# Kernel tuning notes

Hardware: AMD Instinct MI355X
Metric: run time of the kernel (lower is better)

Reference implementation:

```python
import math
import jax, jax.numpy as jnp
import numpy as np

EMB = 1024
HEADS = 16
HD = EMB // HEADS  # 64
MAXPOS = 1024
BATCH = 4
SEQ = 1024


def get_rope_cache(dim, max_pos, theta=10000.0):
    # NOTE: faithfully reproduces the (i - 1) quirk of the source (not the standard i)
    i = jnp.arange(dim // 2, dtype=jnp.float32)
    theta_i = theta ** (-2.0 * (i - 1.0) / dim)
    pos = jnp.arange(max_pos, dtype=jnp.float32)[:, None]
    th = pos * theta_i  # [max_pos, dim//2]
    return jnp.stack([jnp.cos(th), jnp.sin(th)], axis=-1)  # [max_pos, dim//2, 2]


def apply_rope(x, rope_cache):
    # x: [B, H, S, hd]. Source casts pairs to float16 before the complex multiply,
    # then the complex32*complex64 product promotes back to float32 -> emulate via
    # an fp16 round-trip on x, with the rotation itself done in fp32.
    B, H, S, hd = x.shape
    rc = rope_cache[:S]  # [S, hd//2, 2]
    xp = x.reshape(B, H, S, hd // 2, 2).astype(jnp.float16).astype(jnp.float32)
    a, b = xp[..., 0], xp[..., 1]
    cos, sin = rc[..., 0], rc[..., 1]
    rot = jnp.stack([a * cos - b * sin, a * sin + b * cos], axis=-1)
    return rot.reshape(B, H, S, hd)


def setup_inputs() -> dict:
    key = jax.random.key(0)
    ks = jax.random.split(key, 5)
    std = math.sqrt(2.0 / (EMB + EMB))
    x = jax.random.normal(ks[0], (BATCH, SEQ, EMB), dtype=jnp.float32)
    padding_mask = jnp.ones((BATCH, SEQ), dtype=jnp.float32)
    Wq = jax.random.normal(ks[1], (EMB, EMB), dtype=jnp.float32) * std
    Wk = jax.random.normal(ks[2], (EMB, EMB), dtype=jnp.float32) * std
    Wv = jax.random.normal(ks[3], (EMB, EMB), dtype=jnp.float32) * std
    Wo = jax.random.normal(ks[4], (EMB, EMB), dtype=jnp.float32) * std
    rope_cache = get_rope_cache(HD, MAXPOS)
    return {"x": x, "padding_mask": padding_mask, "Wq": Wq, "Wk": Wk,
            "Wv": Wv, "Wo": Wo, "rope_cache": rope_cache}


def reference(x, padding_mask, Wq, Wk, Wv, Wo, rope_cache):
    B, S, E = x.shape

    def heads(t):  # [B,S,E] -> [B,H,S,hd]
        return t.reshape(B, S, HEADS, HD).transpose(0, 2, 1, 3)

    q = heads(x @ Wq.T)
    k = heads(x @ Wk.T)
    v = heads(x @ Wv.T)
    q = apply_rope(q, rope_cache)
    k = apply_rope(k, rope_cache)

    scores = jnp.einsum('bhqd,bhkd->bhqk', q, k)  # [B,H,S,S]
    causal = jnp.tril(jnp.ones((S, S), jnp.float32))
    mask = (causal[None, :, :] * padding_mask[:, None, :])[:, None]  # [B,1,S,S]
    scores = jnp.where(mask == 0, jnp.float32(-1e9), scores) / math.sqrt(HD)
    weights = jax.nn.softmax(scores, axis=-1)

    out = jnp.einsum('bhqk,bhkd->bhqd', weights, v)  # [B,H,S,hd]
    # Faithful to source: transpose(-2,-1) then .view(B,S,-1) scrambles head_dim/seq
    out = out.transpose(0, 1, 3, 2).reshape(B, S, E)
    return out @ Wo.T
```

## Files before the change

kernel.cpp:

```cpp
#include <hip/hip_runtime.h>

#define SEQ   1024
#define HEADS 16
#define HD    64
#define BATCH 4
#define EMB   1024

typedef __attribute__((ext_vector_type(8))) short  short8;
typedef __attribute__((ext_vector_type(4))) float  floatx4;

__device__ __forceinline__ unsigned short f2bf(float f) {
    unsigned u = __builtin_bit_cast(unsigned, f);
    u += 0x7FFF + ((u >> 16) & 1);
    return (unsigned short)(u >> 16);
}

__device__ __forceinline__ void g2l16(const void* g, void* l) {
    __builtin_amdgcn_global_load_lds((const __attribute__((address_space(1))) unsigned int*)g,
                                     (__attribute__((address_space(3))) unsigned int*)l,
                                     16, 0, 0);
}

__device__ __forceinline__ short8 ldsfrag(const unsigned short* base, int row, int cq) {
    int ch = cq ^ (row & 7);
    return *(const short8*)(base + row * 64 + ch * 8);
}

__global__ __launch_bounds__(256) void cvt_kernel(
    const float* __restrict__ x,  const float* __restrict__ wq,
    const float* __restrict__ wk, const float* __restrict__ wv,
    const float* __restrict__ wo,
    unsigned short* __restrict__ xb,  unsigned short* __restrict__ wqb,
    unsigned short* __restrict__ wkb, unsigned short* __restrict__ wvb,
    unsigned short* __restrict__ wob) {
    int blk = blockIdx.x;
    const float* src; unsigned short* dst; int rel;
    if      (blk < 4096) { src = x;  dst = xb;  rel = blk; }
    else if (blk < 5120) { src = wq; dst = wqb; rel = blk - 4096; }
    else if (blk < 6144) { src = wk; dst = wkb; rel = blk - 5120; }
    else if (blk < 7168) { src = wv; dst = wvb; rel = blk - 6144; }
    else                 { src = wo; dst = wob; rel = blk - 7168; }
    size_t i = (size_t)rel * 1024 + threadIdx.x * 4;
    float4 v = *(const float4*)(src + i);
    ushort4 o;
    o.x = f2bf(v.x); o.y = f2bf(v.y); o.z = f2bf(v.z); o.w = f2bf(v.w);
    *(ushort4*)(dst + i) = o;
}

template<int MODE>
__global__ __launch_bounds__(256) void gemm_m97(
    const unsigned short* __restrict__ A, const unsigned short* __restrict__ W,
    void* __restrict__ out0, void* __restrict__ out1, void* __restrict__ out2,
    const float* __restrict__ rc, int M, int N, int K) {
    __shared__ unsigned short As[128 * 64];
    __shared__ unsigned short Bs[128 * 64];
    const int tid  = threadIdx.x;
    const int lane = tid & 63;
    const int wid  = tid >> 6;
    const int l15  = lane & 15, quad = lane >> 4;
    const int wm   = (wid & 1) * 64, wn = (wid >> 1) * 64;
    const int m0   = blockIdx.y * 128, n0 = blockIdx.x * 128;
    const int boff = tid * 16;

    floatx4 acc[4][4] = {};
    const char* Ab = (const char*)A;
    const char* Wb = (const char*)W;
    const size_t rstride = (size_t)K * 2;

    for (int k0 = 0; k0 < K; k0 += 64) {
#pragma unroll
        for (int c = 0; c < 4; c++) {
            int o = c * 4096 + boff;
            int row = o >> 7;
            int sw  = ((o >> 4) & 7) ^ (row & 7);
            g2l16(Ab + (size_t)(m0 + row) * rstride + (size_t)k0 * 2 + sw * 16, (char*)As + o);
            g2l16(Wb + (size_t)(n0 + row) * rstride + (size_t)k0 * 2 + sw * 16, (char*)Bs + o);
        }
        __syncthreads();
#pragma unroll
        for (int ks = 0; ks < 2; ks++) {
            short8 a[4], b[4];
#pragma unroll
            for (int i = 0; i < 4; i++) a[i] = ldsfrag(As, wm + i * 16 + l15, ks * 4 + quad);
#pragma unroll
            for (int j = 0; j < 4; j++) b[j] = ldsfrag(Bs, wn + j * 16 + l15, ks * 4 + quad);
#pragma unroll
            for (int i = 0; i < 4; i++)
#pragma unroll
                for (int j = 0; j < 4; j++)
                    acc[i][j] = __builtin_amdgcn_mfma_f32_16x16x32_bf16(a[i], b[j], acc[i][j], 0, 0, 0);
        }
        __syncthreads();
    }

    const int which = n0 >> 10;
#pragma unroll
    for (int i = 0; i < 4; i++) {
#pragma unroll
        for (int r = 0; r < 4; r++) {
            int m = m0 + wm + i * 16 + quad * 4 + r;
            int bb = m >> 10, s = m & 1023;
#pragma unroll
            for (int j = 0; j < 4; j++) {
                int n = n0 + wn + j * 16 + l15;
                float v = acc[i][j][r];
                if (MODE == 0) {
                    ((float*)out0)[(size_t)m * N + n] = v;
                } else {
                    int nr = n & 1023, h = nr >> 6, d = nr & 63;
                    if (which < 2) {
                        float vp = __shfl_xor(v, 1);
                        float2 cs = *(const float2*)&rc[(size_t)s * 64 + (d & ~1)];
                        v = (l15 & 1) ? (vp * cs.y + v * cs.x) : (v * cs.x - vp * cs.y);
                        unsigned short* dst = (which == 0) ? (unsigned short*)out0
                                                           : (unsigned short*)out1;
                        dst[(((size_t)bb * HEADS + h) * SEQ + s) * HD + d] = f2bf(v);
                    } else {
                        ((unsigned short*)out2)[(((size_t)bb * HEADS + h) * HD + d) * SEQ + s] = f2bf(v);
                    }
                }
            }
        }
    }
}

__global__ __launch_bounds__(256) void attn_kernel(
    const unsigned short* __restrict__ Qb, const unsigned short* __restrict__ Kb,
    const unsigned short* __restrict__ VTb, const float* __restrict__ pm,
    unsigned short* __restrict__ Tb) {
    __shared__ unsigned short Ks[64 * 64];
    __shared__ unsigned short Vs[64 * 64];
    __shared__ unsigned short Ps[4][16][72];
    __shared__ float pmf[64];
    const int tid  = threadIdx.x;
    const int lane = tid & 63, wid = tid >> 6;
    const int l15  = lane & 15, quad = lane >> 4;
    const int bh   = blockIdx.x, b = bh >> 4;
    const int q0   = (15 - blockIdx.y) * 64;
    const int qw   = q0 + wid * 16;
    const int q    = qw + l15;
    const unsigned short* Qh  = Qb  + (size_t)bh * SEQ * HD;
    const unsigned short* Kh  = Kb  + (size_t)bh * SEQ * HD;
    const unsigned short* VTh = VTb + (size_t)bh * HD * SEQ;
    unsigned short*       Th  = Tb  + (size_t)bh * HD * SEQ;
    const float* pmb = pm + b * SEQ;
    const float SCL2 = 0.125f * 1.44269504088896340736f;

    short8 qf0 = *(const short8*)&Qh[(size_t)q * HD + quad * 8];
    short8 qf1 = *(const short8*)&Qh[(size_t)q * HD + 32 + quad * 8];

    floatx4 ot[4] = {};
    float l_lane = 0.f;
    unsigned short (*Pw)[72] = Ps[wid];
    const int boff = tid * 16;

    for (int kvc = 0; kvc <= q0; kvc += 64) {
        const char* kg = (const char*)(Kh + (size_t)kvc * HD);
        const char* vg = (const char*)(VTh + kvc);
#pragma unroll
        for (int c = 0; c < 2; c++) {
            int o = c * 4096 + boff;
            int row = o >> 7;
            int sw  = ((o >> 4) & 7) ^ (row & 7);
            g2l16(kg + (size_t)row * 128 + sw * 16, (char*)Ks + o);
            g2l16(vg + (size_t)row * (SEQ * 2) + sw * 16, (char*)Vs + o);
        }
        if (tid < 64) pmf[tid] = (pmb[kvc + tid] != 0.f) ? 1.f : 0.f;
        __syncthreads();

        const bool diag = (kvc + 63 > qw);
        floatx4 sc[4];
#pragma unroll
        for (int st = 0; st < 4; st++) {
            short8 ka0 = ldsfrag(Ks, st * 16 + l15, quad);
            short8 ka1 = ldsfrag(Ks, st * 16 + l15, 4 + quad);
            floatx4 z = {0.f, 0.f, 0.f, 0.f};
            z = __builtin_amdgcn_mfma_f32_16x16x32_bf16(ka0, qf0, z, 0, 0, 0);
            z = __builtin_amdgcn_mfma_f32_16x16x32_bf16(ka1, qf1, z, 0, 0, 0);
            sc[st] = z;
        }
#pragma unroll
        for (int st = 0; st < 4; st++) {
            float4 pmv = *(const float4*)&pmf[st * 16 + quad * 4];
            int kvbase = kvc + st * 16 + quad * 4;
            ushort4 pk;
#pragma unroll
            for (int r = 0; r < 4; r++) {
                float e = exp2f(sc[st][r] * SCL2) * ((&pmv.x)[r]);
                if (diag && (kvbase + r > q)) e = 0.f;
                l_lane += e;
                (&pk.x)[r] = f2bf(e);
            }
            *(ushort4*)&Pw[l15][st * 16 + quad * 4] = pk;
        }
        asm volatile("s_waitcnt lgkmcnt(0)" ::: "memory");
        short8 pf0 = *(const short8*)&Pw[l15][quad * 8];
        short8 pf1 = *(const short8*)&Pw[l15][32 + quad * 8];

#pragma unroll
        for (int jt = 0; jt < 4; jt++) {
            short8 v0 = ldsfrag(Vs, jt * 16 + l15, quad);
            short8 v1 = ldsfrag(Vs, jt * 16 + l15, 4 + quad);
            ot[jt] = __builtin_amdgcn_mfma_f32_16x16x32_bf16(v0, pf0, ot[jt], 0, 0, 0);
            ot[jt] = __builtin_amdgcn_mfma_f32_16x16x32_bf16(v1, pf1, ot[jt], 0, 0, 0);
        }
        __syncthreads();
    }

    float l = l_lane;
    l += __shfl_xor(l, 16);
    l += __shfl_xor(l, 32);
    float inv = 1.0f / l;
#pragma unroll
    for (int jt = 0; jt < 4; jt++)
#pragma unroll
        for (int r = 0; r < 4; r++)
            Th[(size_t)(jt * 16 + quad * 4 + r) * SEQ + q] = f2bf(ot[jt][r] * inv);
}

extern "C" void kernel_launch(void* const* d_in, const int* in_sizes, int n_in,
                              void* d_out, int out_size, void* d_ws, size_t ws_size,
                              hipStream_t stream) {
    const float* x  = (const float*)d_in[0];
    const float* pm = (const float*)d_in[1];
    const float* Wq = (const float*)d_in[2];
    const float* Wk = (const float*)d_in[3];
    const float* Wv = (const float*)d_in[4];
    const float* Wo = (const float*)d_in[5];
    const float* rc = (const float*)d_in[6];

    char* base = (char*)d_ws;
    unsigned short* xb   = (unsigned short*)(base);
    unsigned short* wqkv = (unsigned short*)(base + (8u  << 20));
    unsigned short* wob  = (unsigned short*)(base + (14u << 20));
    unsigned short* Qb   = (unsigned short*)(base + (16u << 20));
    unsigned short* Kb   = (unsigned short*)(base + (24u << 20));
    unsigned short* VTb  = (unsigned short*)(base + (32u << 20));
    unsigned short* Tb   = (unsigned short*)(base + (40u << 20));

    cvt_kernel<<<8192, 256, 0, stream>>>(x, Wq, Wk, Wv, Wo,
                                         xb, wqkv, wqkv + (1u << 20), wqkv + (2u << 20), wob);
    gemm_m97<1><<<dim3(24, 32), 256, 0, stream>>>(xb, wqkv, (void*)Qb, (void*)Kb, (void*)VTb,
                                                  rc, 4096, 3072, 1024);
    attn_kernel<<<dim3(64, 16), 256, 0, stream>>>(Qb, Kb, VTb, pm, Tb);
    gemm_m97<0><<<dim3(8, 32), 256, 0, stream>>>(Tb, wob, d_out, nullptr, nullptr,
                                                 nullptr, 4096, 1024, 1024);
}
```

Measured before the change: 183.4 us.

## Replace QKV GEMM with 256x256 tile, 8-wave ping-pong pipelined kernel

Adds a dedicated QKV projection kernel that uses 256x256 output tiles, 512 threads and double-buffered LDS. It interleaves async global-to-LDS staging with MFMA phases under explicit barriers, waitcnts and s_setprio. The goal is to hide load latency and raise data reuse relative to the old 128-tile gemm. The cost is a large LDS footprint (128KB per block) and only 192 blocks, which may underfill the GPU; the hand-ordered barrier schedule is also fragile. The old templated gemm stays in use for the output projection only.

Measured after the change: 197.0 us. +7.5%, slower.

```diff
diff --git a/kernel.cpp b/kernel.cpp
--- a/kernel.cpp
+++ b/kernel.cpp
@@ -93,9 +93,140 @@
         __syncthreads();
     }
 
+#pragma unroll
+    for (int i = 0; i < 4; i++) {
+#pragma unroll
+        for (int r = 0; r < 4; r++) {
+            int m = m0 + wm + i * 16 + quad * 4 + r;
+#pragma unroll
+            for (int j = 0; j < 4; j++) {
+                int n = n0 + wn + j * 16 + l15;
+                ((float*)out0)[(size_t)m * N + n] = acc[i][j][r];
+            }
+        }
+    }
+}
+
+__global__ __launch_bounds__(512, 2) void gemm8p_qkv(
+    const unsigned short* __restrict__ A, const unsigned short* __restrict__ W,
+    unsigned short* __restrict__ outQ, unsigned short* __restrict__ outK,
+    unsigned short* __restrict__ outV, const float* __restrict__ rc,
+    int M, int N, int K) {
+    __shared__ unsigned short As[2][256 * 64];
+    __shared__ unsigned short Bs[2][256 * 64];
+    const int tid  = threadIdx.x;
+    const int lane = tid & 63;
+    const int wid  = tid >> 6;
+    const int l15  = lane & 15, quad = lane >> 4;
+    const int wm   = (wid & 1) * 128, wn = (wid >> 1) * 64;
+    const int m0   = blockIdx.y * 256, n0 = blockIdx.x * 256;
+    const int rr   = tid >> 3;
+    const int sw16 = ((tid & 7) ^ (rr & 7)) * 16;
+    const size_t rstride = (size_t)K * 2;
+    const char* baseA = (const char*)A + (size_t)(m0 + rr) * rstride + sw16;
+    const char* baseB = (const char*)W + (size_t)(n0 + rr) * rstride + sw16;
+    const int NT = K >> 6;
+
+    floatx4 acc[8][4] = {};
+    short8 af[4][2], bf[4][2];
+
+    auto stage = [&](const char* g, int h, int kt, unsigned short* buf) {
+#pragma unroll
+        for (int r = 0; r < 2; r++) {
+            int ro = (r << 7) + (h << 6);
+            g2l16(g + (size_t)ro * rstride + ((size_t)kt << 7),
+                  (char*)buf + ro * 128 + tid * 16);
+        }
+    };
+    auto lda = [&](const unsigned short* Asb, int ih) {
+#pragma unroll
+        for (int i = 0; i < 4; i++)
+#pragma unroll
+            for (int s = 0; s < 2; s++)
+                af[i][s] = ldsfrag(Asb, wm + ih * 64 + i * 16 + l15, s * 4 + quad);
+    };
+    auto ldb = [&](const unsigned short* Bsb, int jh) {
+#pragma unroll
+        for (int j = 0; j < 2; j++)
+#pragma unroll
+            for (int s = 0; s < 2; s++)
+                bf[jh * 2 + j][s] = ldsfrag(Bsb, wn + jh * 32 + j * 16 + l15, s * 4 + quad);
+    };
+    auto mfma8 = [&](int ih, int jh) {
+        __builtin_amdgcn_s_setprio(1);
+#pragma unroll
+        for (int i = 0; i < 4; i++)
+#pragma unroll
+            for (int j = 0; j < 2; j++)
+#pragma unroll
+                for (int s = 0; s < 2; s++)
+                    acc[ih * 4 + i][jh * 2 + j] = __builtin_amdgcn_mfma_f32_16x16x32_bf16(
+                        af[i][s], bf[jh * 2 + j][s], acc[ih * 4 + i][jh * 2 + j], 0, 0, 0);
+        __builtin_amdgcn_s_setprio(0);
+    };
+
+    stage(baseA, 0, 0, As[0]); stage(baseA, 1, 0, As[0]);
+    stage(baseB, 0, 0, Bs[0]); stage(baseB, 1, 0, Bs[0]);
+    stage(baseA, 0, 1, As[1]);
+    stage(baseB, 0, 1, Bs[1]); stage(baseB, 1, 1, Bs[1]);
+    asm volatile("s_waitcnt vmcnt(6)" ::: "memory");
+    __builtin_amdgcn_s_barrier();
+
+    for (int t = 0; t < NT / 2; t++) {
+        const int kB = 2 * t + 1;
+        const int s2 = (2 * t + 2) & (NT - 1);
+        const int s3 = (2 * t + 3) & (NT - 1);
+        lda(As[0], 0); ldb(Bs[0], 0);
+        stage(baseA, 1, kB, As[1]);
+        __builtin_amdgcn_s_barrier();
+        asm volatile("s_waitcnt lgkmcnt(0)" ::: "memory");
+        mfma8(0, 0);
+        __builtin_amdgcn_s_barrier();
+        ldb(Bs[0], 1);
+        stage(baseA, 0, s2, As[0]);
+        __builtin_amdgcn_s_barrier();
+        asm volatile("s_waitcnt lgkmcnt(0)" ::: "memory");
+        mfma8(0, 1);
+        __builtin_amdgcn_s_barrier();
+        lda(As[0], 1);
+        stage(baseB, 0, s2, Bs[0]);
+        __builtin_amdgcn_s_barrier();
+        asm volatile("s_waitcnt lgkmcnt(0)" ::: "memory");
+        mfma8(1, 0);
+        __builtin_amdgcn_s_barrier();
+        stage(baseB, 1, s2, Bs[0]);
+        asm volatile("s_waitcnt vmcnt(6)" ::: "memory");
+        __builtin_amdgcn_s_barrier();
+        mfma8(1, 1);
+        __builtin_amdgcn_s_barrier();
+        lda(As[1], 0); ldb(Bs[1], 0);
+        stage(baseA, 1, s2, As[0]);
+        __builtin_amdgcn_s_barrier();
+        asm volatile("s_waitcnt lgkmcnt(0)" ::: "memory");
+        mfma8(0, 0);
+        __builtin_amdgcn_s_barrier();
+        ldb(Bs[1], 1);
+        stage(baseA, 0, s3, As[1]);
+        __builtin_amdgcn_s_barrier();
+        asm volatile("s_waitcnt lgkmcnt(0)" ::: "memory");
+        mfma8(0, 1);
+        __builtin_amdgcn_s_barrier();
+        lda(As[1], 1);
+        stage(baseB, 0, s3, Bs[1]);
+        __builtin_amdgcn_s_barrier();
+        asm volatile("s_waitcnt lgkmcnt(0)" ::: "memory");
+        mfma8(1, 0);
+        __builtin_amdgcn_s_barrier();
+        stage(baseB, 1, s3, Bs[1]);
+        asm volatile("s_waitcnt vmcnt(6)" ::: "memory");
+        __builtin_amdgcn_s_barrier();
+        mfma8(1, 1);
+        __builtin_amdgcn_s_barrier();
+    }
+
     const int which = n0 >> 10;
 #pragma unroll
-    for (int i = 0; i < 4; i++) {
+    for (int i = 0; i < 8; i++) {
 #pragma unroll
         for (int r = 0; r < 4; r++) {
             int m = m0 + wm + i * 16 + quad * 4 + r;
@@ -104,20 +235,15 @@
             for (int j = 0; j < 4; j++) {
                 int n = n0 + wn + j * 16 + l15;
                 float v = acc[i][j][r];
-                if (MODE == 0) {
-                    ((float*)out0)[(size_t)m * N + n] = v;
+                int nr = n & 1023, h = nr >> 6, d = nr & 63;
+                if (which < 2) {
+                    float vp = __shfl_xor(v, 1);
+                    float2 cs = *(const float2*)&rc[(size_t)s * 64 + (d & ~1)];
+                    v = (l15 & 1) ? (vp * cs.y + v * cs.x) : (v * cs.x - vp * cs.y);
+                    unsigned short* dst = (which == 0) ? outQ : outK;
+                    dst[(((size_t)bb * HEADS + h) * SEQ + s) * HD + d] = f2bf(v);
                 } else {
-                    int nr = n & 1023, h = nr >> 6, d = nr & 63;
-                    if (which < 2) {
-                        float vp = __shfl_xor(v, 1);
-                        float2 cs = *(const float2*)&rc[(size_t)s * 64 + (d & ~1)];
-                        v = (l15 & 1) ? (vp * cs.y + v * cs.x) : (v * cs.x - vp * cs.y);
-                        unsigned short* dst = (which == 0) ? (unsigned short*)out0
-                                                           : (unsigned short*)out1;
-                        dst[(((size_t)bb * HEADS + h) * SEQ + s) * HD + d] = f2bf(v);
-                    } else {
-                        ((unsigned short*)out2)[(((size_t)bb * HEADS + h) * HD + d) * SEQ + s] = f2bf(v);
-                    }
+                    outV[(((size_t)bb * HEADS + h) * HD + d) * SEQ + s] = f2bf(v);
                 }
             }
         }
@@ -240,8 +366,8 @@
 
     cvt_kernel<<<8192, 256, 0, stream>>>(x, Wq, Wk, Wv, Wo,
                                          xb, wqkv, wqkv + (1u << 20), wqkv + (2u << 20), wob);
-    gemm_m97<1><<<dim3(24, 32), 256, 0, stream>>>(xb, wqkv, (void*)Qb, (void*)Kb, (void*)VTb,
-                                                  rc, 4096, 3072, 1024);
+    gemm8p_qkv<<<dim3(12, 16), 512, 0, stream>>>(xb, wqkv, Qb, Kb, VTb,
+                                                 rc, 4096, 3072, 1024);
     attn_kernel<<<dim3(64, 16), 256, 0, stream>>>(Qb, Kb, VTb, pm, Tb);
     gemm_m97<0><<<dim3(8, 32), 256, 0, stream>>>(Tb, wob, d_out, nullptr, nullptr,
                                                  nullptr, 4096, 1024, 1024);
```
